# Optimization experiments

Measured on AMD Instinct MI355X. Metric: run time of the kernel, lower is better.

Reference implementation:

```python
import jax, jax.numpy as jnp
import numpy as np

EPS = 1e-5

def bn_feat(x, g, b, m, v):
    # BatchNorm1d over (B, F) in eval mode
    return (x - m) / jnp.sqrt(v + EPS) * g + b

def bn_ch(x, g, b, m, v):
    # BatchNorm1d over (B, C, N) in eval mode, per-channel
    inv = (g / jnp.sqrt(v + EPS))[None, :, None]
    return (x - m[None, :, None]) * inv + b[None, :, None]

def conv1(x, w):
    # 1x1 Conv1d without bias: (O,C) x (B,C,N) -> (B,O,N)
    return jnp.einsum('oc,bcn->bon', w, x)


def setup_inputs() -> dict:
    key = jax.random.key(0)
    ks = iter(jax.random.split(key, 48))
    rn = lambda shape, s=0.05: jax.random.normal(next(ks), shape, dtype=jnp.float32) * s
    ru = lambda shape: jax.random.uniform(next(ks), shape, dtype=jnp.float32) + 0.5
    B, M = 32, 2048
    inp = {
        'global_f': jax.random.normal(next(ks), (B, 512, M), dtype=jnp.float32),
        'latent_w': rn((128, 512)), 'latent_b': rn((128,)),
        'token_w': rn((65536, 512)), 'token_b': rn((65536,)),
        'tbn_g': ru((65536,)), 'tbn_b': rn((65536,)), 'tbn_m': rn((65536,)), 'tbn_v': ru((65536,)),
        'q_w': rn((122, 64)), 'qbn_g': ru((122,)), 'qbn_b': rn((122,)), 'qbn_m': rn((122,)), 'qbn_v': ru((122,)),
        'k_w': rn((122, 64)), 'kbn_g': ru((122,)), 'kbn_b': rn((122,)), 'kbn_m': rn((122,)), 'kbn_v': ru((122,)),
        'v_w': rn((122, 64)), 'vbn_g': ru((122,)), 'vbn_b': rn((122,)), 'vbn_m': rn((122,)), 'vbn_v': ru((122,)),
        'f_w': rn((61, 122)), 'fbn_g': ru((61,)), 'fbn_b': rn((61,)), 'fbn_m': rn((61,)), 'fbn_v': ru((61,)),
        'c1_w': rn((256, 61)), 'c1_b': rn((256,)),
        'c2_w': rn((64, 256)), 'c2_b': rn((64,)),
        'c3_w': rn((3, 64)), 'c3_b': rn((3,)),
    }
    return inp


def reference(global_f, latent_w, latent_b, token_w, token_b, tbn_g, tbn_b, tbn_m, tbn_v,
              q_w, qbn_g, qbn_b, qbn_m, qbn_v, k_w, kbn_g, kbn_b, kbn_m, kbn_v,
              v_w, vbn_g, vbn_b, vbn_m, vbn_v, f_w, fbn_g, fbn_b, fbn_m, fbn_v,
              c1_w, c1_b, c2_w, c2_b, c3_w, c3_b):
    B = global_f.shape[0]
    # encoder max-pool: (B,512,M) -> (B,512)
    gfeat = jnp.max(global_f, axis=2)
    # ITSI: latent is computed in torch forward but discarded
    _latent = gfeat @ latent_w.T + latent_b
    tok = gfeat @ token_w.T + token_b                 # (B, 64*1024)
    tok = jax.nn.relu(bn_feat(tok, tbn_g, tbn_b, tbn_m, tbn_v))
    tok = tok.reshape(B, 64, 1024)                    # (B, C=64, N=1024)
    # SelfAttentionUnit (softmax-free)
    q = jax.nn.relu(bn_ch(conv1(tok, q_w), qbn_g, qbn_b, qbn_m, qbn_v))   # (B,122,1024)
    k = jax.nn.relu(bn_ch(conv1(tok, k_w), kbn_g, kbn_b, kbn_m, kbn_v))
    v = jax.nn.relu(bn_ch(conv1(tok, v_w), vbn_g, vbn_b, vbn_m, vbn_v))
    attn = jnp.einsum('bcn,bcm->bnm', q, k)           # Q^T K : (B,1024,1024)
    val = jnp.einsum('bnm,bcm->bcn', attn, v)         # (A V^T)^T : (B,122,1024)
    fused = jax.nn.relu(bn_ch(conv1(val, f_w), fbn_g, fbn_b, fbn_m, fbn_v))  # (B,61,1024)
    h = jax.nn.relu(conv1(fused, c1_w) + c1_b[None, :, None])
    h = jax.nn.relu(conv1(h, c2_w) + c2_b[None, :, None])
    o = jax.nn.sigmoid(conv1(h, c3_w) + c3_b[None, :, None])   # (B,3,1024)
    o = o * 1.0 - 0.5                                  # range_max=0.5: o*0.5*2 - 0.5
    return jnp.transpose(o, (0, 2, 1))                 # (B,1024,3)
```

## Files before the change

kernel.cpp:

```cpp
#include <hip/hip_runtime.h>
#include <float.h>

#define EPS 1e-5f
#define FMA4(A_, W_, T_) { (A_).x += (W_)*(T_).x; (A_).y += (W_)*(T_).y; (A_).z += (W_)*(T_).z; (A_).w += (W_)*(T_).w; }

__global__ __launch_bounds__(256) void k1_maxpool(const float* __restrict__ gf, float* __restrict__ gfeat) {
    int row = blockIdx.x * 4 + (threadIdx.x >> 6);
    int lane = threadIdx.x & 63;
    const float4* p = (const float4*)(gf + (size_t)row * 2048);
    float m = -FLT_MAX;
#pragma unroll
    for (int w = 0; w < 8; ++w) {
        float4 v = p[lane + (w << 6)];
        m = fmaxf(m, fmaxf(fmaxf(v.x, v.y), fmaxf(v.z, v.w)));
    }
#pragma unroll
    for (int off = 32; off >= 1; off >>= 1) m = fmaxf(m, __shfl_xor(m, off));
    if (lane == 0) gfeat[row] = m;
}

__global__ __launch_bounds__(256) void k2_token(
    const float* __restrict__ gfeat, const float* __restrict__ tw, const float* __restrict__ tbias,
    const float* __restrict__ bg, const float* __restrict__ bb,
    const float* __restrict__ bm, const float* __restrict__ bv,
    float* __restrict__ tok) {
    __shared__ __align__(16) float wl[128 * 33];
    __shared__ __align__(16) float gl[32 * 36];
    int tid = threadIdx.x;
    int t0 = blockIdx.x * 128;
    int tx = tid & 7, ty = tid >> 3;
    float4 acc[4];
#pragma unroll
    for (int i = 0; i < 4; ++i) acc[i] = make_float4(0.f, 0.f, 0.f, 0.f);
    for (int k0 = 0; k0 < 512; k0 += 32) {
        if (k0) __syncthreads();
        {
            int r = tid >> 1, h = tid & 1;
            const float* src = tw + (size_t)(t0 + r) * 512 + k0 + h * 16;
            float* dst = wl + r * 33 + h * 16;
#pragma unroll
            for (int q = 0; q < 4; ++q) {
                float4 x = *(const float4*)(src + q * 4);
                dst[q*4+0] = x.x; dst[q*4+1] = x.y; dst[q*4+2] = x.z; dst[q*4+3] = x.w;
            }
            int bq = tid >> 3, kq = tid & 7;
            float4 gx = *(const float4*)(gfeat + bq * 512 + k0 + kq * 4);
            gl[(kq*4+0)*36 + bq] = gx.x;
            gl[(kq*4+1)*36 + bq] = gx.y;
            gl[(kq*4+2)*36 + bq] = gx.z;
            gl[(kq*4+3)*36 + bq] = gx.w;
        }
        __syncthreads();
#pragma unroll
        for (int kk = 0; kk < 32; ++kk) {
            float4 g4 = *(const float4*)(gl + kk * 36 + tx * 4);
#pragma unroll
            for (int i = 0; i < 4; ++i) {
                float a = wl[(ty * 4 + i) * 33 + kk];
                FMA4(acc[i], a, g4);
            }
        }
    }
#pragma unroll
    for (int i = 0; i < 4; ++i) {
        int t = t0 + ty * 4 + i;
        float scale = bg[t] * rsqrtf(bv[t] + EPS);
        float sh = (tbias[t] - bm[t]) * scale + bb[t];
        tok[(size_t)(tx*4+0) * 65536 + t] = fmaxf(acc[i].x * scale + sh, 0.f);
        tok[(size_t)(tx*4+1) * 65536 + t] = fmaxf(acc[i].y * scale + sh, 0.f);
        tok[(size_t)(tx*4+2) * 65536 + t] = fmaxf(acc[i].z * scale + sh, 0.f);
        tok[(size_t)(tx*4+3) * 65536 + t] = fmaxf(acc[i].w * scale + sh, 0.f);
    }
}

__global__ __launch_bounds__(256) void k3_kv(
    const float* __restrict__ tok,
    const float* __restrict__ kw, const float* __restrict__ vw,
    const float* __restrict__ kg, const float* __restrict__ kb, const float* __restrict__ km, const float* __restrict__ kvv,
    const float* __restrict__ vg, const float* __restrict__ vb, const float* __restrict__ vm, const float* __restrict__ vvv,
    float* __restrict__ kbuf, float* __restrict__ vbuf) {
    __shared__ __align__(16) float tokt[64 * 68];
    int tid = threadIdx.x;
    int b = blockIdx.y;
    int n0 = blockIdx.x << 6;
    for (int i = tid; i < 1024; i += 256) {
        int c = i >> 4, q4 = i & 15;
        float4 x = *(const float4*)(tok + (size_t)b * 65536 + c * 1024 + n0 + q4 * 4);
        tokt[(q4*4+0)*68 + c] = x.x;
        tokt[(q4*4+1)*68 + c] = x.y;
        tokt[(q4*4+2)*68 + c] = x.z;
        tokt[(q4*4+3)*68 + c] = x.w;
    }
    int o = tid & 127;
    bool valid = (o < 122);
    float kscl = 0.f, kshf = 0.f, vscl = 0.f, vshf = 0.f;
    if (valid) {
        float s = kg[o] * rsqrtf(kvv[o] + EPS);
        kscl = s; kshf = kb[o] - km[o] * s;
        s = vg[o] * rsqrtf(vvv[o] + EPS);
        vscl = s; vshf = vb[o] - vm[o] * s;
    }
    float4 kwreg[16], vwreg[16];
    {
        const float* kwr = kw + o * 64;
        const float* vwr = vw + o * 64;
#pragma unroll
        for (int c4 = 0; c4 < 16; ++c4) {
            kwreg[c4] = valid ? *(const float4*)(kwr + c4 * 4) : make_float4(0.f,0.f,0.f,0.f);
            vwreg[c4] = valid ? *(const float4*)(vwr + c4 * 4) : make_float4(0.f,0.f,0.f,0.f);
        }
    }
    __syncthreads();
    for (int nn = (tid >> 7); nn < 64; nn += 2) {
        const float* t = tokt + nn * 68;
        float sk = 0.f, sv = 0.f;
#pragma unroll
        for (int c4 = 0; c4 < 16; ++c4) {
            float4 tv = *(const float4*)(t + c4 * 4);
            sk += kwreg[c4].x*tv.x + kwreg[c4].y*tv.y + kwreg[c4].z*tv.z + kwreg[c4].w*tv.w;
            sv += vwreg[c4].x*tv.x + vwreg[c4].y*tv.y + vwreg[c4].z*tv.z + vwreg[c4].w*tv.w;
        }
        size_t base = ((size_t)b * 1024 + n0 + nn) * 128 + o;
        kbuf[base] = fmaxf(sk * kscl + kshf, 0.f);
        vbuf[base] = fmaxf(sv * vscl + vshf, 0.f);
    }
}

__global__ __launch_bounds__(256) void k3_q(
    const float* __restrict__ tok,
    const float* __restrict__ qw,
    const float* __restrict__ qg, const float* __restrict__ qb, const float* __restrict__ qm, const float* __restrict__ qv,
    float* __restrict__ qbuf) {
    __shared__ __align__(16) float tokt[64 * 68];
    int tid = threadIdx.x;
    int b = blockIdx.y;
    int n0 = blockIdx.x << 6;
    for (int i = tid; i < 1024; i += 256) {
        int c = i >> 4, q4 = i & 15;
        float4 x = *(const float4*)(tok + (size_t)b * 65536 + c * 1024 + n0 + q4 * 4);
        tokt[(q4*4+0)*68 + c] = x.x;
        tokt[(q4*4+1)*68 + c] = x.y;
        tokt[(q4*4+2)*68 + c] = x.z;
        tokt[(q4*4+3)*68 + c] = x.w;
    }
    int o = tid & 127;
    bool valid = (o < 122);
    float scl = 0.f, shf = 0.f;
    if (valid) {
        float s = qg[o] * rsqrtf(qv[o] + EPS);
        scl = s; shf = qb[o] - qm[o] * s;
    }
    float4 wreg[16];
    {
        const float* wr = qw + o * 64;
#pragma unroll
        for (int c4 = 0; c4 < 16; ++c4)
            wreg[c4] = valid ? *(const float4*)(wr + c4 * 4) : make_float4(0.f,0.f,0.f,0.f);
    }
    __syncthreads();
    for (int nn = (tid >> 7); nn < 64; nn += 2) {
        const float* t = tokt + nn * 68;
        float s = 0.f;
#pragma unroll
        for (int c4 = 0; c4 < 16; ++c4) {
            float4 tv = *(const float4*)(t + c4 * 4);
            s += wreg[c4].x*tv.x + wreg[c4].y*tv.y + wreg[c4].z*tv.z + wreg[c4].w*tv.w;
        }
        qbuf[((size_t)b * 1024 + n0 + nn) * 128 + o] = fmaxf(s * scl + shf, 0.f);
    }
}

__global__ __launch_bounds__(256) void k4_s(
    const float* __restrict__ kbuf, const float* __restrict__ vbuf,
    float* __restrict__ sp) {
    __shared__ __align__(16) float kl[32 * 128];
    __shared__ __align__(16) float vl[32 * 128];
    int tid = threadIdx.x;
    int b = blockIdx.y, ns = blockIdx.x;
    int tx = tid & 15, ty = tid >> 4;
    float acc[8][8];
#pragma unroll
    for (int i = 0; i < 8; ++i)
#pragma unroll
        for (int j = 0; j < 8; ++j) acc[i][j] = 0.f;
    for (int chunk = 0; chunk < 2; ++chunk) {
        int nb = (ns << 6) + (chunk << 5);
        if (chunk) __syncthreads();
        for (int i = tid; i < 1024; i += 256) {
            int n = i >> 5, q = i & 31;
            size_t src = ((size_t)b * 1024 + nb + n) * 128 + q * 4;
            *(float4*)(kl + n * 128 + q * 4) = *(const float4*)(kbuf + src);
            *(float4*)(vl + n * 128 + q * 4) = *(const float4*)(vbuf + src);
        }
        __syncthreads();
        for (int n = 0; n < 32; ++n) {
            const float* kr = kl + n * 128 + ty * 8;
            const float* vr = vl + n * 128 + tx * 8;
            float4 ka = *(const float4*)(kr),  kb4 = *(const float4*)(kr + 4);
            float4 va = *(const float4*)(vr),  vb4 = *(const float4*)(vr + 4);
            float av[8]  = {ka.x,ka.y,ka.z,ka.w,kb4.x,kb4.y,kb4.z,kb4.w};
            float bvv[8] = {va.x,va.y,va.z,va.w,vb4.x,vb4.y,vb4.z,vb4.w};
#pragma unroll
            for (int i = 0; i < 8; ++i)
#pragma unroll
                for (int j = 0; j < 8; ++j) acc[i][j] += av[i] * bvv[j];
        }
    }
    size_t sbase = ((size_t)(b * 16 + ns)) << 14;
#pragma unroll
    for (int i = 0; i < 8; ++i) {
        int cp = ty * 8 + i;
        *(float4*)(sp + sbase + (cp << 7) + tx * 8)     = make_float4(acc[i][0], acc[i][1], acc[i][2], acc[i][3]);
        *(float4*)(sp + sbase + (cp << 7) + tx * 8 + 4) = make_float4(acc[i][4], acc[i][5], acc[i][6], acc[i][7]);
    }
}

__global__ __launch_bounds__(256) void k4b_reduce(const float* __restrict__ sp, float* __restrict__ spad) {
    int idx = blockIdx.x * 256 + threadIdx.x;
    if (idx >= 32 * 122 * 128) return;
    int c = idx & 127;
    int r = (idx >> 7) % 122;
    int b = idx / (122 * 128);
    float s = 0.f;
    if (c < 122) {
        const float* p = sp + (((size_t)b * 16) << 14) + (r << 7) + c;
#pragma unroll
        for (int q = 0; q < 16; ++q) s += p[(size_t)q << 14];
    }
    spad[idx] = s;
}

__global__ __launch_bounds__(256) void k5_tail(
    const float* __restrict__ qbuf,
    const float* __restrict__ spad,
    const float* __restrict__ fw, const float* __restrict__ fg, const float* __restrict__ fbb,
    const float* __restrict__ fm, const float* __restrict__ fv,
    const float* __restrict__ w1, const float* __restrict__ bb1,
    const float* __restrict__ w2, const float* __restrict__ bb2,
    const float* __restrict__ w3, const float* __restrict__ bb3,
    float* __restrict__ out) {
    __shared__ __align__(16) float lds[6096];
    const int VAL = 2560, FUS = 0, H1 = 976, H2 = 5072;
    int tid = threadIdx.x;
    int b = blockIdx.y;
    int n0 = blockIdx.x << 4;
    int nq = tid & 3, og = tid >> 2;
    for (int i = tid; i < 512; i += 256) {
        int n = i >> 5, c4 = i & 31;
        float4 x = *(const float4*)(qbuf + ((size_t)b * 1024 + n0 + n) * 128 + c4 * 4);
        lds[(c4*4+0)*20 + n] = x.x;
        lds[(c4*4+1)*20 + n] = x.y;
        lds[(c4*4+2)*20 + n] = x.z;
        lds[(c4*4+3)*20 + n] = x.w;
    }
    __syncthreads();
    {
        float4 a0 = make_float4(0,0,0,0), a1 = a0;
        const float* sb = spad + (size_t)b * 15616 + og * 2;
        for (int cp = 0; cp < 122; ++cp) {
            float4 tv = *(const float4*)(lds + cp * 20 + nq * 4);
            float2 s2 = *(const float2*)(sb + cp * 128);
            FMA4(a0, s2.x, tv); FMA4(a1, s2.y, tv);
        }
        __syncthreads();
        *(float4*)(lds + VAL + (og*2+0)*20 + nq*4) = a0;
        *(float4*)(lds + VAL + (og*2+1)*20 + nq*4) = a1;
        __syncthreads();
    }
    {
        float4 y = make_float4(0.f, 0.f, 0.f, 0.f);
        const bool act = (og < 61);
        if (act) {
            float4 a0 = make_float4(0,0,0,0);
            const float* fwr = fw + og * 122;
            for (int cp = 0; cp < 122; ++cp) {
                float4 tv = *(const float4*)(lds + VAL + cp*20 + nq*4);
                FMA4(a0, fwr[cp], tv);
            }
            float sc = fg[og] * rsqrtf(fv[og] + EPS);
            float sh = fbb[og] - fm[og] * sc;
            y.x = fmaxf(a0.x*sc+sh, 0.f); y.y = fmaxf(a0.y*sc+sh, 0.f);
            y.z = fmaxf(a0.z*sc+sh, 0.f); y.w = fmaxf(a0.w*sc+sh, 0.f);
        }
        __syncthreads();
        if (act) *(float4*)(lds + FUS + og*16 + nq*4) = y;
        __syncthreads();
    }
    {
        float4 a[4];
#pragma unroll
        for (int i = 0; i < 4; ++i) a[i] = make_float4(0,0,0,0);
        for (int c = 0; c < 61; ++c) {
            float4 tv = *(const float4*)(lds + FUS + c*16 + nq*4);
#pragma unroll
            for (int i = 0; i < 4; ++i) {
                float w = w1[(og + (i<<6)) * 61 + c];
                FMA4(a[i], w, tv);
            }
        }
#pragma unroll
        for (int i = 0; i < 4; ++i) {
            int o = og + (i<<6);
            float bias = bb1[o];
            float4 y;
            y.x = fmaxf(a[i].x + bias, 0.f); y.y = fmaxf(a[i].y + bias, 0.f);
            y.z = fmaxf(a[i].z + bias, 0.f); y.w = fmaxf(a[i].w + bias, 0.f);
            *(float4*)(lds + H1 + o*16 + nq*4) = y;
        }
        __syncthreads();
    }
    {
        float4 a0 = make_float4(0,0,0,0);
        const float* w2r = w2 + og * 256;
        for (int c = 0; c < 256; ++c) {
            float4 tv = *(const float4*)(lds + H1 + c*16 + nq*4);
            FMA4(a0, w2r[c], tv);
        }
        float ba = bb2[og];
        float4 y;
        y.x = fmaxf(a0.x + ba, 0.f); y.y = fmaxf(a0.y + ba, 0.f);
        y.z = fmaxf(a0.z + ba, 0.f); y.w = fmaxf(a0.w + ba, 0.f);
        *(float4*)(lds + H2 + og*16 + nq*4) = y;
        __syncthreads();
    }
    if (og < 3) {
        float4 a = make_float4(0,0,0,0);
        const float* w3r = w3 + og * 64;
        for (int c = 0; c < 64; ++c) {
            float4 tv = *(const float4*)(lds + H2 + c*16 + nq*4);
            FMA4(a, w3r[c], tv);
        }
        float bias = bb3[og];
        int nbase = n0 + nq*4;
        out[((size_t)b*1024 + nbase + 0)*3 + og] = 1.f/(1.f+expf(-(a.x+bias))) - 0.5f;
        out[((size_t)b*1024 + nbase + 1)*3 + og] = 1.f/(1.f+expf(-(a.y+bias))) - 0.5f;
        out[((size_t)b*1024 + nbase + 2)*3 + og] = 1.f/(1.f+expf(-(a.z+bias))) - 0.5f;
        out[((size_t)b*1024 + nbase + 3)*3 + og] = 1.f/(1.f+expf(-(a.w+bias))) - 0.5f;
    }
}

extern "C" void kernel_launch(void* const* d_in, const int* in_sizes, int n_in,
                              void* d_out, int out_size, void* d_ws, size_t ws_size,
                              hipStream_t stream) {
    const float* gf      = (const float*)d_in[0];
    const float* token_w = (const float*)d_in[3];
    const float* token_b = (const float*)d_in[4];
    const float* tbn_g   = (const float*)d_in[5];
    const float* tbn_b   = (const float*)d_in[6];
    const float* tbn_m   = (const float*)d_in[7];
    const float* tbn_v   = (const float*)d_in[8];
    const float* q_w = (const float*)d_in[9];
    const float* qg  = (const float*)d_in[10];
    const float* qb  = (const float*)d_in[11];
    const float* qm  = (const float*)d_in[12];
    const float* qv  = (const float*)d_in[13];
    const float* k_w = (const float*)d_in[14];
    const float* kg  = (const float*)d_in[15];
    const float* kb  = (const float*)d_in[16];
    const float* km  = (const float*)d_in[17];
    const float* kv  = (const float*)d_in[18];
    const float* v_w = (const float*)d_in[19];
    const float* vg  = (const float*)d_in[20];
    const float* vb  = (const float*)d_in[21];
    const float* vm  = (const float*)d_in[22];
    const float* vv  = (const float*)d_in[23];
    const float* f_w = (const float*)d_in[24];
    const float* fg  = (const float*)d_in[25];
    const float* fb  = (const float*)d_in[26];
    const float* fm  = (const float*)d_in[27];
    const float* fv  = (const float*)d_in[28];
    const float* c1w = (const float*)d_in[29];
    const float* c1b = (const float*)d_in[30];
    const float* c2w = (const float*)d_in[31];
    const float* c2b = (const float*)d_in[32];
    const float* c3w = (const float*)d_in[33];
    const float* c3b = (const float*)d_in[34];

    float* ws    = (float*)d_ws;
    float* gfeat = ws;
    float* tok   = gfeat + 16384;
    float* kbuf  = tok   + 2097152;
    float* vbuf  = kbuf  + 4194304;
    float* qbuf  = vbuf  + 4194304;
    float* sp    = qbuf  + 4194304;
    float* spad  = sp    + 8388608;

    k1_maxpool<<<4096, 256, 0, stream>>>(gf, gfeat);
    k2_token  <<<512, 256, 0, stream>>>(gfeat, token_w, token_b, tbn_g, tbn_b, tbn_m, tbn_v, tok);
    k3_kv     <<<dim3(16, 32), 256, 0, stream>>>(tok, k_w, v_w,
                 kg, kb, km, kv, vg, vb, vm, vv, kbuf, vbuf);
    k3_q      <<<dim3(16, 32), 256, 0, stream>>>(tok, q_w, qg, qb, qm, qv, qbuf);
    k4_s      <<<dim3(16, 32), 256, 0, stream>>>(kbuf, vbuf, sp);
    k4b_reduce<<<1952, 256, 0, stream>>>(sp, spad);
    k5_tail   <<<dim3(64, 32), 256, 0, stream>>>(qbuf, spad,
                 f_w, fg, fb, fm, fv, c1w, c1b, c2w, c2b, c3w, c3b, (float*)d_out);
}
```

Before: 301.0 us.

## Fold fuse-conv weights and BN scale into per-batch attention matrix

Adds a small per-batch kernel that multiplies the fuse conv weights (61x122) by the per-batch K·V^T summary matrix and pre-applies the BN scale. The tail kernel then does one 122->61 contraction on Q instead of two chained 122-wide contractions. This removes one LDS stage and its syncs in every tail block. The cost is an extra kernel launch running on only 32 blocks, plus an extra global buffer.

New measurement: 306.3 us. Within noise of the previous version (+1.8%).

```diff
diff --git a/kernel.cpp b/kernel.cpp
--- a/kernel.cpp
+++ b/kernel.cpp
@@ -230,17 +230,38 @@
     spad[idx] = s;
 }
 
+__global__ __launch_bounds__(256) void k4c_fold(
+    const float* __restrict__ spad, const float* __restrict__ fw,
+    const float* __restrict__ fg, const float* __restrict__ fv,
+    float* __restrict__ Tt) {
+    __shared__ __align__(16) float sl[122 * 128];
+    int b = blockIdx.x, tid = threadIdx.x;
+    for (int i = tid; i < 3904; i += 256)
+        *(float4*)(sl + i * 4) = *(const float4*)(spad + (size_t)b * 15616 + i * 4);
+    __syncthreads();
+    int o = tid & 63, cpg = tid >> 6;
+    if (o < 61) {
+        float sc = fg[o] * rsqrtf(fv[o] + EPS);
+        const float* fwr = fw + o * 122;
+        for (int cp = cpg; cp < 122; cp += 4) {
+            const float* sr = sl + cp * 128;
+            float s = 0.f;
+            for (int c = 0; c < 122; ++c) s += fwr[c] * sr[c];
+            Tt[((size_t)b * 122 + cp) * 64 + o] = sc * s;
+        }
+    }
+}
+
 __global__ __launch_bounds__(256) void k5_tail(
-    const float* __restrict__ qbuf,
-    const float* __restrict__ spad,
-    const float* __restrict__ fw, const float* __restrict__ fg, const float* __restrict__ fbb,
+    const float* __restrict__ qbuf, const float* __restrict__ Tt,
+    const float* __restrict__ fg, const float* __restrict__ fbb,
     const float* __restrict__ fm, const float* __restrict__ fv,
     const float* __restrict__ w1, const float* __restrict__ bb1,
     const float* __restrict__ w2, const float* __restrict__ bb2,
     const float* __restrict__ w3, const float* __restrict__ bb3,
     float* __restrict__ out) {
-    __shared__ __align__(16) float lds[6096];
-    const int VAL = 2560, FUS = 0, H1 = 976, H2 = 5072;
+    __shared__ __align__(16) float lds[7560];
+    const int FUS = 0, H1 = 2440, H2 = 6536;
     int tid = threadIdx.x;
     int b = blockIdx.y;
     int n0 = blockIdx.x << 4;
@@ -255,32 +276,19 @@
     }
     __syncthreads();
     {
-        float4 a0 = make_float4(0,0,0,0), a1 = a0;
-        const float* sb = spad + (size_t)b * 15616 + og * 2;
-        for (int cp = 0; cp < 122; ++cp) {
-            float4 tv = *(const float4*)(lds + cp * 20 + nq * 4);
-            float2 s2 = *(const float2*)(sb + cp * 128);
-            FMA4(a0, s2.x, tv); FMA4(a1, s2.y, tv);
-        }
-        __syncthreads();
-        *(float4*)(lds + VAL + (og*2+0)*20 + nq*4) = a0;
-        *(float4*)(lds + VAL + (og*2+1)*20 + nq*4) = a1;
-        __syncthreads();
-    }
-    {
         float4 y = make_float4(0.f, 0.f, 0.f, 0.f);
         const bool act = (og < 61);
         if (act) {
             float4 a0 = make_float4(0,0,0,0);
-            const float* fwr = fw + og * 122;
+            const float* tb = Tt + (size_t)b * 7808 + og;
             for (int cp = 0; cp < 122; ++cp) {
-                float4 tv = *(const float4*)(lds + VAL + cp*20 + nq*4);
-                FMA4(a0, fwr[cp], tv);
+                float4 tv = *(const float4*)(lds + cp * 20 + nq * 4);
+                FMA4(a0, tb[cp << 6], tv);
             }
             float sc = fg[og] * rsqrtf(fv[og] + EPS);
             float sh = fbb[og] - fm[og] * sc;
-            y.x = fmaxf(a0.x*sc+sh, 0.f); y.y = fmaxf(a0.y*sc+sh, 0.f);
-            y.z = fmaxf(a0.z*sc+sh, 0.f); y.w = fmaxf(a0.w*sc+sh, 0.f);
+            y.x = fmaxf(a0.x + sh, 0.f); y.y = fmaxf(a0.y + sh, 0.f);
+            y.z = fmaxf(a0.z + sh, 0.f); y.w = fmaxf(a0.w + sh, 0.f);
         }
         __syncthreads();
         if (act) *(float4*)(lds + FUS + og*16 + nq*4) = y;
@@ -384,6 +392,7 @@
     float* qbuf  = vbuf  + 4194304;
     float* sp    = qbuf  + 4194304;
     float* spad  = sp    + 8388608;
+    float* Tt    = spad  + 499712;
 
     k1_maxpool<<<4096, 256, 0, stream>>>(gf, gfeat);
     k2_token  <<<512, 256, 0, stream>>>(gfeat, token_w, token_b, tbn_g, tbn_b, tbn_m, tbn_v, tok);
@@ -392,6 +401,7 @@
     k3_q      <<<dim3(16, 32), 256, 0, stream>>>(tok, q_w, qg, qb, qm, qv, qbuf);
     k4_s      <<<dim3(16, 32), 256, 0, stream>>>(kbuf, vbuf, sp);
     k4b_reduce<<<1952, 256, 0, stream>>>(sp, spad);
-    k5_tail   <<<dim3(64, 32), 256, 0, stream>>>(qbuf, spad,
-                 f_w, fg, fb, fm, fv, c1w, c1b, c2w, c2b, c3w, c3b, (float*)d_out);
-}
+    k4c_fold  <<<32, 256, 0, stream>>>(spad, f_w, fg, fv, Tt);
+    k5_tail   <<<dim3(64, 32), 256, 0, stream>>>(qbuf, Tt,
+                 fg, fb, fm, fv, c1w, c1b, c2w, c2b, c3w, c3b, (float*)d_out);
+}
```
